# Kernel optimization log

Measured on AMD Instinct MI355X. Metric: run time of the kernel, lower is better.

## Reference

```python
import jax, jax.numpy as jnp
import numpy as np

VOCAB = 49408
D = 768
H = 12
DH = D // H
FF = 3072
L = 4
B = 32
S = 512
EPS = 1e-6


def _pos_encoding(seq_len, d):
    pos = np.arange(seq_len, dtype=np.float64)[:, None]
    j = np.arange(d, dtype=np.float64)[None, :]
    ang = pos / np.power(10000.0, 2.0 * (j // 2) / d)
    pe = np.where((np.arange(d) % 2) == 0, np.sin(ang), np.cos(ang))
    return jnp.asarray(pe, dtype=jnp.float32)  # [seq_len, d]


def _layernorm(x, g, b):
    m = jnp.mean(x, axis=-1, keepdims=True)
    v = jnp.mean(jnp.square(x - m), axis=-1, keepdims=True)
    return g * (x - m) * jax.lax.rsqrt(v + EPS) + b


def setup_inputs() -> dict:
    key = jax.random.key(0)
    ks = jax.random.split(key, 16)
    s = 0.02
    inp = {
        "tokens": jax.random.randint(ks[0], (B, S), 0, VOCAB, dtype=jnp.int32),
        "emb": jax.random.normal(ks[1], (VOCAB, D), jnp.float32) * s,
        "wq": jax.random.normal(ks[2], (L, D, D), jnp.float32) * s,
        "bq": jnp.zeros((L, D), jnp.float32),
        "wk": jax.random.normal(ks[3], (L, D, D), jnp.float32) * s,
        "bk": jnp.zeros((L, D), jnp.float32),
        "wv": jax.random.normal(ks[4], (L, D, D), jnp.float32) * s,
        "bv": jnp.zeros((L, D), jnp.float32),
        "wo": jax.random.normal(ks[5], (L, D, D), jnp.float32) * s,
        "bo": jnp.zeros((L, D), jnp.float32),
        "w1": jax.random.normal(ks[6], (L, D, FF), jnp.float32) * s,
        "b1": jnp.zeros((L, FF), jnp.float32),
        "w2": jax.random.normal(ks[7], (L, FF, D), jnp.float32) * s,
        "b2": jnp.zeros((L, D), jnp.float32),
        "ln1_g": jnp.ones((L, D), jnp.float32),
        "ln1_b": jnp.zeros((L, D), jnp.float32),
        "ln2_g": jnp.ones((L, D), jnp.float32),
        "ln2_b": jnp.zeros((L, D), jnp.float32),
        "wl": jax.random.normal(ks[8], (D, 32), jnp.float32) * s,
        "bl": jnp.zeros((32,), jnp.float32),
        "wout": jax.random.normal(ks[9], (32, 1), jnp.float32) * s,
        "bout": jnp.zeros((1,), jnp.float32),
    }
    return inp


def reference(tokens, emb, wq, bq, wk, bk, wv, bv, wo, bo, w1, b1, w2, b2,
              ln1_g, ln1_b, ln2_g, ln2_b, wl, bl, wout, bout):
    seq_len = tokens.shape[1]
    pe = _pos_encoding(seq_len, D)  # [S, D] constant
    x = emb[tokens] * jnp.sqrt(jnp.float32(D)) + pe[None, :, :]  # [B,S,D]
    scale = 1.0 / jnp.sqrt(jnp.float32(DH))
    for i in range(L):
        # multi-head attention (naive full score matrix, mask=None)
        q = (jnp.einsum('bsd,de->bse', x, wq[i]) + bq[i]).reshape(-1, seq_len, H, DH)
        k = (jnp.einsum('bsd,de->bse', x, wk[i]) + bk[i]).reshape(-1, seq_len, H, DH)
        v = (jnp.einsum('bsd,de->bse', x, wv[i]) + bv[i]).reshape(-1, seq_len, H, DH)
        scores = jnp.einsum('bqhd,bkhd->bhqk', q, k) * scale  # [B,H,S,S]
        attn = jax.nn.softmax(scores, axis=-1)
        av = jnp.einsum('bhqk,bkhd->bqhd', attn, v).reshape(-1, seq_len, D)
        attn_out = jnp.einsum('bsd,de->bse', av, wo[i]) + bo[i]
        out1 = _layernorm(x + attn_out, ln1_g[i], ln1_b[i])
        # FFN: relu -> dense
        h = jax.nn.relu(jnp.einsum('bsd,df->bsf', out1, w1[i]) + b1[i])
        ffn = jnp.einsum('bsf,fd->bsd', h, w2[i]) + b2[i]
        x = _layernorm(out1 + ffn, ln2_g[i], ln2_b[i])
    pooled = jnp.mean(x, axis=1)  # GlobalAveragePooling1D -> [B,D]
    h = jax.nn.gelu(pooled @ wl + bl, approximate=False)
    out = jax.nn.sigmoid(h @ wout + bout)  # [B,1]
    return out
```

## Files before the change

kernel.cpp:

```cpp
#include <hip/hip_runtime.h>
#include <hip/hip_bf16.h>
#include <math.h>


#define B_  32
#define S_  512
#define D_  768
#define H_  12
#define DH_ 64
#define FF_ 3072
#define L_  4
#define QKVSTR 2304

typedef __attribute__((ext_vector_type(8))) short short8;
typedef __attribute__((ext_vector_type(4))) short short4v;
typedef __attribute__((ext_vector_type(4))) float f32x4;

__device__ __forceinline__ void async16(const void* g, void* l) {
    __builtin_amdgcn_global_load_lds(
        (const __attribute__((address_space(1))) void*)g,
        (__attribute__((address_space(3))) void*)l, 16, 0, 0);
}

__device__ __forceinline__ ushort f2bf(float f) {
    __hip_bfloat16 h = __float2bfloat16(f);
    return __builtin_bit_cast(ushort, h);
}

__device__ __forceinline__ short8 scale8_eighth(short8 v) {
    short8 r;
#pragma unroll
    for (int e = 0; e < 8; e++) {
        ushort u = (ushort)v[e];
        ushort ex = u & 0x7f80;
        r[e] = (short)(ex > 0x0180 ? (ushort)(u - 0x0180) : (ushort)(u & 0x8000));
    }
    return r;
}

__global__ void pe_kernel(float* __restrict__ pe) {
    int idx = blockIdx.x * 256 + threadIdx.x;
    if (idx >= S_ * D_) return;
    int s = idx / D_, j = idx % D_;
    double e = (2.0 * (double)(j >> 1)) / (double)D_;
    double denom = pow(10000.0, e);
    double ang = (double)s / denom;
    pe[idx] = (j & 1) ? (float)cos(ang) : (float)sin(ang);
}

__global__ void embed_kernel(const int* __restrict__ tokens,
                             const float* __restrict__ emb,
                             const float* __restrict__ pe,
                             float* __restrict__ x,
                             __hip_bfloat16* __restrict__ xb) {
    int row = blockIdx.x;
    int s = row & (S_ - 1);
    int tok = tokens[row];
    float scale = sqrtf((float)D_);
    for (int i = threadIdx.x; i < D_; i += 256) {
        float v = emb[(size_t)tok * D_ + i] * scale + pe[s * D_ + i];
        x[(size_t)row * D_ + i] = v;
        xb[(size_t)row * D_ + i] = __float2bfloat16(v);
    }
}

__global__ __launch_bounds__(256) void transpose_bf16_l(
    const float* __restrict__ in, __hip_bfloat16* __restrict__ out,
    int R, int C, size_t inL, size_t outL)
{
    __shared__ float tile[32][33];
    in  += (size_t)blockIdx.z * inL;
    out += (size_t)blockIdx.z * outL;
    int tx = threadIdx.x & 31, ty = threadIdx.x >> 5;
    int c0 = blockIdx.x * 32, r0 = blockIdx.y * 32;
#pragma unroll
    for (int d = 0; d < 32; d += 8)
        tile[ty + d][tx] = in[(size_t)(r0 + ty + d) * C + c0 + tx];
    __syncthreads();
#pragma unroll
    for (int d = 0; d < 32; d += 8)
        out[(size_t)(c0 + ty + d) * R + r0 + tx] = __float2bfloat16(tile[tx][ty + d]);
}

__global__ void biascat(const float* __restrict__ bq, const float* __restrict__ bk,
                        const float* __restrict__ bv, float* __restrict__ o) {
    int i = blockIdx.x * 256 + threadIdx.x;
    int ll = i / QKVSTR, j = i % QKVSTR;
    o[i] = j < 768 ? bq[ll * 768 + j]
         : j < 1536 ? bk[ll * 768 + j - 768]
                    : bv[ll * 768 + j - 1536];
}

#define BAR()   __builtin_amdgcn_s_barrier()
#define LGKM0() asm volatile("s_waitcnt lgkmcnt(0)" ::: "memory")
#define VM4()   asm volatile("s_waitcnt vmcnt(4)" ::: "memory")

#define STAGE_A(buf, h, kt) do { \
    async16(aSrc[h][0] + (kt) * 64, &lds[(buf) * 2][dOff[h][0]]); \
    async16(aSrc[h][1] + (kt) * 64, &lds[(buf) * 2][dOff[h][1]]); } while (0)
#define STAGE_B(buf, h, kt) do { \
    async16(bSrc[h][0] + (kt) * 64, &lds[(buf) * 2 + 1][dOff[h][0]]); \
    async16(bSrc[h][1] + (kt) * 64, &lds[(buf) * 2 + 1][dOff[h][1]]); } while (0)

#define LDA(buf, m, ks) (*(const short8*)((const char*)(&lds[(buf) * 2][0]) + \
    (size_t)((arow + (m) * 16) * 128 + cswz[ks])))
#define LDB(buf, n, ks) (*(const short8*)((const char*)(&lds[(buf) * 2 + 1][0]) + \
    (size_t)((brow + (n) * 16) * 128 + cswz[ks])))

#define MFMA_Q(mh, nh) do { \
    __builtin_amdgcn_s_setprio(1); \
    _Pragma("unroll") \
    for (int ks_ = 0; ks_ < 2; ks_++) { \
      _Pragma("unroll") \
      for (int n_ = 0; n_ < 2; n_++) { \
        _Pragma("unroll") \
        for (int m_ = 0; m_ < 4; m_++) { \
          acc[(mh) * 4 + m_][(nh) * 2 + n_] = \
              __builtin_amdgcn_mfma_f32_16x16x32_bf16( \
                  a[m_][ks_], b[(nh) * 2 + n_][ks_], \
                  acc[(mh) * 4 + m_][(nh) * 2 + n_], 0, 0, 0); \
        } } } \
    __builtin_amdgcn_s_setprio(0); \
} while (0)

template<int RELU>
__global__ __launch_bounds__(512, 2) void gemm256(
    const ushort* __restrict__ A,
    const ushort* __restrict__ Bt,
    const float* __restrict__ bias,
    __hip_bfloat16* __restrict__ C,
    int M, int N, int K, int NX)
{
    __shared__ alignas(16) ushort lds[4][16384];

    int t = threadIdx.x;
    int l = t & 63, w = t >> 6;
    int wmi = w >> 2, wni = w & 3;
    int lm = l & 15, lo = l >> 4;

    int nwg = gridDim.x;
    int bid = blockIdx.x;
    int lid = (nwg & 7) ? bid : ((bid & 7) * (nwg >> 3) + (bid >> 3));
    int bn = lid % NX, bm = lid / NX;
    int row0 = bm << 8, col0 = bn << 8;

    const ushort* aSrc[2][2];
    const ushort* bSrc[2][2];
    int dOff[2][2];
#pragma unroll
    for (int h = 0; h < 2; h++) {
#pragma unroll
        for (int c = 0; c < 2; c++) {
            int p = h * 16384 + c * 8192 + t * 16;
            int prow = p >> 7;
            int scolb = (p & 127) ^ ((prow & 7) << 4);
            dOff[h][c] = p >> 1;
            aSrc[h][c] = A  + (size_t)(row0 + prow) * K + (scolb >> 1);
            bSrc[h][c] = Bt + (size_t)(col0 + prow) * K + (scolb >> 1);
        }
    }

    int arow = wmi * 128 + lm;
    int brow = wni * 64 + lm;
    int swz = (lm & 7) << 4;
    int cswz[2];
    cswz[0] = (lo * 16) ^ swz;
    cswz[1] = (64 + lo * 16) ^ swz;

    f32x4 acc[8][4];
#pragma unroll
    for (int i = 0; i < 8; i++)
#pragma unroll
        for (int j = 0; j < 4; j++) acc[i][j] = (f32x4){0.f, 0.f, 0.f, 0.f};
    short8 a[4][2], b[4][2];

    const int NK = K >> 6;
    const int NI = NK >> 1;

    STAGE_A(0, 0, 0); STAGE_A(0, 1, 0);
    STAGE_B(0, 0, 0); STAGE_B(0, 1, 0);
    STAGE_B(1, 0, 1); STAGE_B(1, 1, 1);
    VM4();
    BAR();

    for (int i = 0; i < NI; i++) {
        int kt  = 2 * i;
        int ktA = (kt + 2 <= NK - 2) ? kt + 2 : NK - 2;
        int ktB = (kt + 3 <= NK - 1) ? kt + 3 : NK - 1;

#pragma unroll
        for (int m = 0; m < 4; m++) { a[m][0] = LDA(0, m, 0); a[m][1] = LDA(0, m, 1); }
#pragma unroll
        for (int n = 0; n < 2; n++) { b[n][0] = LDB(0, n, 0); b[n][1] = LDB(0, n, 1); }
        STAGE_A(1, 0, kt + 1);
        BAR(); LGKM0();
        MFMA_Q(0, 0);
        BAR();

#pragma unroll
        for (int n = 0; n < 2; n++) { b[2 + n][0] = LDB(0, 2 + n, 0); b[2 + n][1] = LDB(0, 2 + n, 1); }
        STAGE_A(1, 1, kt + 1);
        BAR(); LGKM0();
        MFMA_Q(0, 1);
        BAR();

#pragma unroll
        for (int m = 0; m < 4; m++) { a[m][0] = LDA(0, 4 + m, 0); a[m][1] = LDA(0, 4 + m, 1); }
        STAGE_B(0, 0, ktA);
        BAR(); LGKM0();
        MFMA_Q(1, 0);
        BAR();

        STAGE_B(0, 1, ktA);
        BAR(); LGKM0();
        MFMA_Q(1, 1);
        VM4();
        BAR();

#pragma unroll
        for (int m = 0; m < 4; m++) { a[m][0] = LDA(1, m, 0); a[m][1] = LDA(1, m, 1); }
#pragma unroll
        for (int n = 0; n < 2; n++) { b[n][0] = LDB(1, n, 0); b[n][1] = LDB(1, n, 1); }
        STAGE_A(0, 0, ktA);
        BAR(); LGKM0();
        MFMA_Q(0, 0);
        BAR();

#pragma unroll
        for (int n = 0; n < 2; n++) { b[2 + n][0] = LDB(1, 2 + n, 0); b[2 + n][1] = LDB(1, 2 + n, 1); }
        STAGE_A(0, 1, ktA);
        BAR(); LGKM0();
        MFMA_Q(0, 1);
        BAR();

#pragma unroll
        for (int m = 0; m < 4; m++) { a[m][0] = LDA(1, 4 + m, 0); a[m][1] = LDA(1, 4 + m, 1); }
        STAGE_B(1, 0, ktB);
        BAR(); LGKM0();
        MFMA_Q(1, 0);
        BAR();

        STAGE_B(1, 1, ktB);
        BAR(); LGKM0();
        MFMA_Q(1, 1);
        VM4();
        BAR();
    }

    int crow = row0 + wmi * 128;
    int ccol = col0 + wni * 64;
#pragma unroll
    for (int n = 0; n < 4; n++) {
        int c = ccol + n * 16 + lm;
        float bs = bias[c];
#pragma unroll
        for (int m = 0; m < 8; m++) {
#pragma unroll
            for (int r = 0; r < 4; r++) {
                float v = acc[m][n][r] + bs;
                if (RELU) v = fmaxf(v, 0.f);
                C[(size_t)(crow + m * 16 + lo * 4 + r) * N + c] = __float2bfloat16(v);
            }
        }
    }
    (void)M;
}

#define PSTR 72
__global__ __launch_bounds__(256) void attn_mfma(
    const ushort* __restrict__ qkv,
    __hip_bfloat16* __restrict__ av)
{
    __shared__ alignas(16) ushort sQP[128 * PSTR];
    __shared__ alignas(16) ushort sK[64 * PSTR];
    __shared__ alignas(16) ushort sVt[64 * PSTR];

    int t = threadIdx.x;
    int qt = blockIdx.x, h = blockIdx.y, b = blockIdx.z;
    int w = t >> 6, l = t & 63;
    int lm = l & 15, lq = l >> 4;
    int wm = w * 32;

    const ushort* qbase = qkv + (size_t)(b * S_ + qt * 128) * QKVSTR + h * DH_;
    const ushort* kbase = qkv + (size_t)b * S_ * QKVSTR + 768 + h * DH_;
    const ushort* vbase = qkv + (size_t)b * S_ * QKVSTR + 1536 + h * DH_;

    {
        int r = t >> 1, c0 = (t & 1) * 32;
        const ushort* src = qbase + (size_t)r * QKVSTR + c0;
        ushort* dst = &sQP[r * PSTR + c0];
        *(uint4*)(dst + 0)  = *(const uint4*)(src + 0);
        *(uint4*)(dst + 8)  = *(const uint4*)(src + 8);
        *(uint4*)(dst + 16) = *(const uint4*)(src + 16);
        *(uint4*)(dst + 24) = *(const uint4*)(src + 24);
    }
    __syncthreads();
    short8 qf[2][2];
#pragma unroll
    for (int i = 0; i < 2; i++)
#pragma unroll
        for (int ks = 0; ks < 2; ks++)
            qf[i][ks] = scale8_eighth(
                *(const short8*)&sQP[(wm + i * 16 + lm) * PSTR + ks * 32 + lq * 8]);

    ushort* sPw = &sQP[(size_t)wm * PSTR];

    f32x4 accO[4][2];
    float mrun[2], lrun[2];
#pragma unroll
    for (int dk = 0; dk < 4; dk++)
#pragma unroll
        for (int i = 0; i < 2; i++) accO[dk][i] = (f32x4){0.f, 0.f, 0.f, 0.f};
    mrun[0] = mrun[1] = -1e30f;
    lrun[0] = lrun[1] = 0.f;

    for (int kt = 0; kt < S_ / 64; kt++) {
        __syncthreads();
        {
            int r = t >> 2, c0 = (t & 3) * 16;
            const ushort* ksrc = kbase + (size_t)(kt * 64 + r) * QKVSTR + c0;
            ushort* kdst = &sK[r * PSTR + c0];
            *(uint4*)(kdst + 0) = *(const uint4*)(ksrc + 0);
            *(uint4*)(kdst + 8) = *(const uint4*)(ksrc + 8);
            int p = t & 31, d0 = (t >> 5) * 8;
            const ushort* vsrc = vbase + (size_t)(kt * 64 + 2 * p) * QKVSTR + d0;
            uint4 v0 = *(const uint4*)(vsrc);
            uint4 v1 = *(const uint4*)(vsrc + QKVSTR);
            const ushort* e0 = (const ushort*)&v0;
            const ushort* e1 = (const ushort*)&v1;
#pragma unroll
            for (int j = 0; j < 8; j++) {
                uint pk = (uint)e0[j] | ((uint)e1[j] << 16);
                *(uint*)&sVt[(d0 + j) * PSTR + 2 * p] = pk;
            }
        }
        __syncthreads();

        f32x4 accS[4][2];
#pragma unroll
        for (int sb = 0; sb < 4; sb++)
#pragma unroll
            for (int i = 0; i < 2; i++) accS[sb][i] = (f32x4){0.f, 0.f, 0.f, 0.f};
#pragma unroll
        for (int ks = 0; ks < 2; ks++) {
#pragma unroll
            for (int sb = 0; sb < 4; sb++) {
                short8 kf = *(const short8*)&sK[(sb * 16 + lm) * PSTR + ks * 32 + lq * 8];
#pragma unroll
                for (int i = 0; i < 2; i++)
                    accS[sb][i] = __builtin_amdgcn_mfma_f32_16x16x32_bf16(
                        kf, qf[i][ks], accS[sb][i], 0, 0, 0);
            }
        }

        float pmax[2];
#pragma unroll
        for (int i = 0; i < 2; i++) {
            float m0 = accS[0][i][0];
#pragma unroll
            for (int sb = 0; sb < 4; sb++)
#pragma unroll
                for (int r = 0; r < 4; r++) m0 = fmaxf(m0, accS[sb][i][r]);
            m0 = fmaxf(m0, __shfl_xor(m0, 16));
            m0 = fmaxf(m0, __shfl_xor(m0, 32));
            pmax[i] = m0;
        }
        float alpha[2];
#pragma unroll
        for (int i = 0; i < 2; i++) {
            float mn = fmaxf(mrun[i], pmax[i]);
            alpha[i] = __expf(mrun[i] - mn);
            mrun[i] = mn;
        }
        float rsum[2] = {0.f, 0.f};
#pragma unroll
        for (int sb = 0; sb < 4; sb++)
#pragma unroll
            for (int i = 0; i < 2; i++)
#pragma unroll
                for (int r = 0; r < 4; r++) {
                    float p = __expf(accS[sb][i][r] - mrun[i]);
                    accS[sb][i][r] = p;
                    rsum[i] += p;
                }
#pragma unroll
        for (int i = 0; i < 2; i++) {
            rsum[i] += __shfl_xor(rsum[i], 16);
            rsum[i] += __shfl_xor(rsum[i], 32);
            lrun[i] = lrun[i] * alpha[i] + rsum[i];
        }

#pragma unroll
        for (int dk = 0; dk < 4; dk++)
#pragma unroll
            for (int i = 0; i < 2; i++)
#pragma unroll
                for (int r = 0; r < 4; r++) accO[dk][i][r] *= alpha[i];

#pragma unroll
        for (int i = 0; i < 2; i++)
#pragma unroll
            for (int sb = 0; sb < 4; sb++) {
                short4v pk;
#pragma unroll
                for (int r = 0; r < 4; r++) pk[r] = (short)f2bf(accS[sb][i][r]);
                *(short4v*)&sPw[(i * 16 + lm) * PSTR + sb * 16 + lq * 4] = pk;
            }

#pragma unroll
        for (int ks = 0; ks < 2; ks++) {
            short8 pf[2];
#pragma unroll
            for (int i = 0; i < 2; i++)
                pf[i] = *(const short8*)&sPw[(i * 16 + lm) * PSTR + ks * 32 + lq * 8];
#pragma unroll
            for (int dk = 0; dk < 4; dk++) {
                short8 vf = *(const short8*)&sVt[(dk * 16 + lm) * PSTR + ks * 32 + lq * 8];
#pragma unroll
                for (int i = 0; i < 2; i++)
                    accO[dk][i] = __builtin_amdgcn_mfma_f32_16x16x32_bf16(
                        vf, pf[i], accO[dk][i], 0, 0, 0);
            }
        }
    }

    float invl[2];
    invl[0] = 1.0f / lrun[0];
    invl[1] = 1.0f / lrun[1];
#pragma unroll
    for (int i = 0; i < 2; i++) {
        int row = qt * 128 + wm + i * 16 + lm;
        __hip_bfloat16* dst = av + (size_t)(b * S_ + row) * D_ + h * DH_;
#pragma unroll
        for (int dk = 0; dk < 4; dk++) {
            short4v ok;
#pragma unroll
            for (int r = 0; r < 4; r++) ok[r] = (short)f2bf(accO[dk][i][r] * invl[i]);
            *(short4v*)(dst + dk * 16 + lq * 4) = ok;
        }
    }
}

__global__ __launch_bounds__(256) void add_ln(float* __restrict__ x,
    __hip_bfloat16* __restrict__ xb,
    const __hip_bfloat16* __restrict__ r, const float* __restrict__ g,
    const float* __restrict__ bta)
{
    __shared__ float sred[256];
    int row = blockIdx.x, t = threadIdx.x;
    size_t base = (size_t)row * D_;
    float v0 = x[base + t]       + __bfloat162float(r[base + t]);
    float v1 = x[base + t + 256] + __bfloat162float(r[base + t + 256]);
    float v2 = x[base + t + 512] + __bfloat162float(r[base + t + 512]);
    sred[t] = v0 + v1 + v2;
    __syncthreads();
    for (int o = 128; o > 0; o >>= 1) { if (t < o) sred[t] += sred[t + o]; __syncthreads(); }
    float mean = sred[0] * (1.0f / D_);
    __syncthreads();
    float d0 = v0 - mean, d1 = v1 - mean, d2 = v2 - mean;
    sred[t] = d0 * d0 + d1 * d1 + d2 * d2;
    __syncthreads();
    for (int o = 128; o > 0; o >>= 1) { if (t < o) sred[t] += sred[t + o]; __syncthreads(); }
    float rstd = rsqrtf(sred[0] * (1.0f / D_) + 1e-6f);
    float o0 = g[t]       * d0 * rstd + bta[t];
    float o1 = g[t + 256] * d1 * rstd + bta[t + 256];
    float o2 = g[t + 512] * d2 * rstd + bta[t + 512];
    x[base + t]       = o0;
    x[base + t + 256] = o1;
    x[base + t + 512] = o2;
    xb[base + t]       = __float2bfloat16(o0);
    xb[base + t + 256] = __float2bfloat16(o1);
    xb[base + t + 512] = __float2bfloat16(o2);
}

__global__ void pool_kernel(const float* __restrict__ x, float* __restrict__ pooled) {
    int idx = blockIdx.x * 256 + threadIdx.x;
    int b = idx / D_, d = idx % D_;
    float acc = 0.f;
    const float* p = x + (size_t)b * S_ * D_ + d;
    for (int s = 0; s < S_; s++) acc += p[(size_t)s * D_];
    pooled[idx] = acc * (1.0f / S_);
}

__global__ void head_kernel(const float* __restrict__ pooled,
                            const float* __restrict__ wl,
                            const float* __restrict__ bl,
                            const float* __restrict__ wout,
                            const float* __restrict__ bout,
                            float* __restrict__ out)
{
    __shared__ float hb[32];
    int b = blockIdx.x, t = threadIdx.x;
    if (t < 32) {
        float z = bl[t];
        for (int d = 0; d < D_; d++) z += pooled[b * D_ + d] * wl[d * 32 + t];
        hb[t] = 0.5f * z * (1.0f + erff(z * 0.70710678118654752f));
    }
    __syncthreads();
    if (t == 0) {
        float z = bout[0];
        for (int j = 0; j < 32; j++) z += hb[j] * wout[j];
        out[b] = 1.0f / (1.0f + expf(-z));
    }
}

extern "C" void kernel_launch(void* const* d_in, const int* in_sizes, int n_in,
                              void* d_out, int out_size, void* d_ws, size_t ws_size,
                              hipStream_t stream)
{
    (void)in_sizes; (void)n_in; (void)out_size; (void)ws_size;
    const int*   tokens = (const int*)  d_in[0];
    const float* emb    = (const float*)d_in[1];
    const float* wq     = (const float*)d_in[2];
    const float* bq     = (const float*)d_in[3];
    const float* wk     = (const float*)d_in[4];
    const float* bk     = (const float*)d_in[5];
    const float* wv     = (const float*)d_in[6];
    const float* bv     = (const float*)d_in[7];
    const float* wo     = (const float*)d_in[8];
    const float* bo     = (const float*)d_in[9];
    const float* w1     = (const float*)d_in[10];
    const float* b1     = (const float*)d_in[11];
    const float* w2     = (const float*)d_in[12];
    const float* b2     = (const float*)d_in[13];
    const float* ln1g   = (const float*)d_in[14];
    const float* ln1b   = (const float*)d_in[15];
    const float* ln2g   = (const float*)d_in[16];
    const float* ln2b   = (const float*)d_in[17];
    const float* wl     = (const float*)d_in[18];
    const float* bl     = (const float*)d_in[19];
    const float* wout   = (const float*)d_in[20];
    const float* bout   = (const float*)d_in[21];
    float* out = (float*)d_out;

    char* ws = (char*)d_ws;
    size_t off = 0;
    auto alloc = [&](size_t n) -> void* {
        char* p = ws + off;
        off = (off + n + 255) & ~(size_t)255;
        return (void*)p;
    };
    const size_t XBYTES = (size_t)B_ * S_ * D_ * 4;
    const size_t XBF    = XBYTES / 2;
    float*          pe     = (float*)alloc((size_t)S_ * D_ * 4);
    float*          x      = (float*)alloc(XBYTES);
    __hip_bfloat16* xb     = (__hip_bfloat16*)alloc(XBF);
    __hip_bfloat16* r_bf   = (__hip_bfloat16*)alloc(XBF);
    char*           arena  = (char*)alloc(4 * XBF);
    __hip_bfloat16* qkv_bf = (__hip_bfloat16*)arena;
    __hip_bfloat16* av_bf  = (__hip_bfloat16*)(arena + 3 * XBF);
    __hip_bfloat16* h_bf   = (__hip_bfloat16*)arena;
    __hip_bfloat16* wT     = (__hip_bfloat16*)alloc((size_t)L_ * 7077888 * 2);
    float*          qkvbias= (float*)alloc((size_t)L_ * QKVSTR * 4);
    float*          pooled = (float*)alloc((size_t)B_ * D_ * 4);

    const int M = B_ * S_;
    const size_t DD = (size_t)D_ * D_;
    const size_t DF = (size_t)D_ * FF_;
    const size_t LSTRIDE = 4 * DD + 2 * DF;

    transpose_bf16_l<<<dim3(D_ / 32, D_ / 32, L_), 256, 0, stream>>>(
        wq, wT + 0 * DD, D_, D_, DD, LSTRIDE);
    transpose_bf16_l<<<dim3(D_ / 32, D_ / 32, L_), 256, 0, stream>>>(
        wk, wT + 1 * DD, D_, D_, DD, LSTRIDE);
    transpose_bf16_l<<<dim3(D_ / 32, D_ / 32, L_), 256, 0, stream>>>(
        wv, wT + 2 * DD, D_, D_, DD, LSTRIDE);
    transpose_bf16_l<<<dim3(D_ / 32, D_ / 32, L_), 256, 0, stream>>>(
        wo, wT + 3 * DD, D_, D_, DD, LSTRIDE);
    transpose_bf16_l<<<dim3(FF_ / 32, D_ / 32, L_), 256, 0, stream>>>(
        w1, wT + 4 * DD, D_, FF_, DF, LSTRIDE);
    transpose_bf16_l<<<dim3(D_ / 32, FF_ / 32, L_), 256, 0, stream>>>(
        w2, wT + 4 * DD + DF, FF_, D_, DF, LSTRIDE);
    biascat<<<(L_ * QKVSTR) / 256, 256, 0, stream>>>(bq, bk, bv, qkvbias);

    pe_kernel<<<(S_ * D_ + 255) / 256, 256, 0, stream>>>(pe);
    embed_kernel<<<M, 256, 0, stream>>>(tokens, emb, pe, x, xb);

    for (int l = 0; l < L_; l++) {
        __hip_bfloat16* wl_base = wT + (size_t)l * LSTRIDE;
        const ushort* qkvT = (const ushort*)(wl_base + 0 * DD);
        const ushort* woT  = (const ushort*)(wl_base + 3 * DD);
        const ushort* w1T  = (const ushort*)(wl_base + 4 * DD);
        const ushort* w2T  = (const ushort*)(wl_base + 4 * DD + DF);

        gemm256<0><<<dim3((QKVSTR / 256) * (M / 256)), 512, 0, stream>>>(
            (const ushort*)xb, qkvT, qkvbias + (size_t)l * QKVSTR, qkv_bf,
            M, QKVSTR, D_, QKVSTR / 256);

        attn_mfma<<<dim3(S_ / 128, H_, B_), 256, 0, stream>>>(
            (const ushort*)qkv_bf, av_bf);

        gemm256<0><<<dim3((D_ / 256) * (M / 256)), 512, 0, stream>>>(
            (const ushort*)av_bf, woT, bo + l * D_, r_bf, M, D_, D_, D_ / 256);
        add_ln<<<M, 256, 0, stream>>>(x, xb, r_bf, ln1g + l * D_, ln1b + l * D_);

        gemm256<1><<<dim3((FF_ / 256) * (M / 256)), 512, 0, stream>>>(
            (const ushort*)xb, w1T, b1 + l * FF_, h_bf, M, FF_, D_, FF_ / 256);
        gemm256<0><<<dim3((D_ / 256) * (M / 256)), 512, 0, stream>>>(
            (const ushort*)h_bf, w2T, b2 + l * D_, r_bf, M, D_, FF_, D_ / 256);
        add_ln<<<M, 256, 0, stream>>>(x, xb, r_bf, ln2g + l * D_, ln2b + l * D_);
    }

    pool_kernel<<<(B_ * D_) / 256, 256, 0, stream>>>(x, pooled);
    head_kernel<<<B_, 64, 0, stream>>>(pooled, wl, bl, wout, bout, out);
}
```

Measured before the change: 1.963 ms.

## Drop fp32 residual stream and stage GEMM epilogue through LDS for coalesced stores

Removes the fp32 copy of the residual activation x, keeping only the bf16 copy, so add_ln, embed and pooling read and write half the bytes. add_ln now loads packed bf16 pairs and writes bf16 in place. The GEMM epilogue writes the tile into LDS and then stores 16-byte coalesced rows instead of scattered 2-byte stores. This needs a full vmcnt(0) wait before the epilogue, and keeping the residual in bf16 lowers its precision across layers.

```diff
diff --git a/kernel.cpp b/kernel.cpp
--- a/kernel.cpp
+++ b/kernel.cpp
@@ -26,6 +26,8 @@
     __hip_bfloat16 h = __float2bfloat16(f);
     return __builtin_bit_cast(ushort, h);
 }
+__device__ __forceinline__ float bflo(uint u) { return __uint_as_float(u << 16); }
+__device__ __forceinline__ float bfhi(uint u) { return __uint_as_float(u & 0xffff0000u); }
 
 __device__ __forceinline__ short8 scale8_eighth(short8 v) {
     short8 r;
@@ -51,7 +53,6 @@
 __global__ void embed_kernel(const int* __restrict__ tokens,
                              const float* __restrict__ emb,
                              const float* __restrict__ pe,
-                             float* __restrict__ x,
                              __hip_bfloat16* __restrict__ xb) {
     int row = blockIdx.x;
     int s = row & (S_ - 1);
@@ -59,7 +60,6 @@
     float scale = sqrtf((float)D_);
     for (int i = threadIdx.x; i < D_; i += 256) {
         float v = emb[(size_t)tok * D_ + i] * scale + pe[s * D_ + i];
-        x[(size_t)row * D_ + i] = v;
         xb[(size_t)row * D_ + i] = __float2bfloat16(v);
     }
 }
@@ -94,6 +94,7 @@
 #define BAR()   __builtin_amdgcn_s_barrier()
 #define LGKM0() asm volatile("s_waitcnt lgkmcnt(0)" ::: "memory")
 #define VM4()   asm volatile("s_waitcnt vmcnt(4)" ::: "memory")
+#define VM0()   asm volatile("s_waitcnt vmcnt(0)" ::: "memory")
 
 #define STAGE_A(buf, h, kt) do { \
     async16(aSrc[h][0] + (kt) * 64, &lds[(buf) * 2][dOff[h][0]]); \
@@ -243,25 +244,37 @@
         STAGE_B(1, 1, ktB);
         BAR(); LGKM0();
         MFMA_Q(1, 1);
-        VM4();
-        BAR();
-    }
-
-    int crow = row0 + wmi * 128;
-    int ccol = col0 + wni * 64;
-#pragma unroll
-    for (int n = 0; n < 4; n++) {
-        int c = ccol + n * 16 + lm;
-        float bs = bias[c];
-#pragma unroll
-        for (int m = 0; m < 8; m++) {
-#pragma unroll
-            for (int r = 0; r < 4; r++) {
-                float v = acc[m][n][r] + bs;
-                if (RELU) v = fmaxf(v, 0.f);
-                C[(size_t)(crow + m * 16 + lo * 4 + r) * N + c] = __float2bfloat16(v);
+        VM0();
+        BAR();
+    }
+
+    ushort* eL = &lds[0][0];
+    {
+        int crow = wmi * 128;
+        int ccol = wni * 64;
+#pragma unroll
+        for (int n = 0; n < 4; n++) {
+            int c = ccol + n * 16 + lm;
+            float bs = bias[col0 + c];
+#pragma unroll
+            for (int m = 0; m < 8; m++) {
+#pragma unroll
+                for (int r = 0; r < 4; r++) {
+                    float v = acc[m][n][r] + bs;
+                    if (RELU) v = fmaxf(v, 0.f);
+                    eL[(crow + m * 16 + lo * 4 + r) * 256 + c] = f2bf(v);
+                }
             }
         }
+    }
+    __syncthreads();
+#pragma unroll
+    for (int i = 0; i < 16; i++) {
+        int byteoff = i * 8192 + t * 16;
+        int rr = byteoff >> 9;
+        int cc = (byteoff & 511) >> 1;
+        uint4 v = *(const uint4*)((const char*)eL + byteoff);
+        *(uint4*)(C + (size_t)(row0 + rr) * N + col0 + cc) = v;
     }
     (void)M;
 }
@@ -441,44 +454,58 @@
     }
 }
 
-__global__ __launch_bounds__(256) void add_ln(float* __restrict__ x,
+__global__ __launch_bounds__(256) void add_ln(
     __hip_bfloat16* __restrict__ xb,
     const __hip_bfloat16* __restrict__ r, const float* __restrict__ g,
     const float* __restrict__ bta)
 {
     __shared__ float sred[256];
     int row = blockIdx.x, t = threadIdx.x;
-    size_t base = (size_t)row * D_;
-    float v0 = x[base + t]       + __bfloat162float(r[base + t]);
-    float v1 = x[base + t + 256] + __bfloat162float(r[base + t + 256]);
-    float v2 = x[base + t + 512] + __bfloat162float(r[base + t + 512]);
-    sred[t] = v0 + v1 + v2;
+    uint* xu = (uint*)(xb + (size_t)row * D_);
+    const uint* ru = (const uint*)(r + (size_t)row * D_);
+    uint ux0 = xu[t], ur0 = ru[t];
+    float a0 = bflo(ux0) + bflo(ur0);
+    float a1 = bfhi(ux0) + bfhi(ur0);
+    float a2 = 0.f, a3 = 0.f;
+    if (t < 128) {
+        uint ux1 = xu[256 + t], ur1 = ru[256 + t];
+        a2 = bflo(ux1) + bflo(ur1);
+        a3 = bfhi(ux1) + bfhi(ur1);
+    }
+    sred[t] = a0 + a1 + a2 + a3;
     __syncthreads();
     for (int o = 128; o > 0; o >>= 1) { if (t < o) sred[t] += sred[t + o]; __syncthreads(); }
     float mean = sred[0] * (1.0f / D_);
     __syncthreads();
-    float d0 = v0 - mean, d1 = v1 - mean, d2 = v2 - mean;
-    sred[t] = d0 * d0 + d1 * d1 + d2 * d2;
+    float d0 = a0 - mean, d1 = a1 - mean;
+    float d2 = a2 - mean, d3 = a3 - mean;
+    sred[t] = d0 * d0 + d1 * d1 + (t < 128 ? d2 * d2 + d3 * d3 : 0.f);
     __syncthreads();
     for (int o = 128; o > 0; o >>= 1) { if (t < o) sred[t] += sred[t + o]; __syncthreads(); }
     float rstd = rsqrtf(sred[0] * (1.0f / D_) + 1e-6f);
-    float o0 = g[t]       * d0 * rstd + bta[t];
-    float o1 = g[t + 256] * d1 * rstd + bta[t + 256];
-    float o2 = g[t + 512] * d2 * rstd + bta[t + 512];
-    x[base + t]       = o0;
-    x[base + t + 256] = o1;
-    x[base + t + 512] = o2;
-    xb[base + t]       = __float2bfloat16(o0);
-    xb[base + t + 256] = __float2bfloat16(o1);
-    xb[base + t + 512] = __float2bfloat16(o2);
-}
-
-__global__ void pool_kernel(const float* __restrict__ x, float* __restrict__ pooled) {
+    {
+        float2 gv = ((const float2*)g)[t];
+        float2 bv = ((const float2*)bta)[t];
+        float o0 = gv.x * d0 * rstd + bv.x;
+        float o1 = gv.y * d1 * rstd + bv.y;
+        xu[t] = (uint)f2bf(o0) | ((uint)f2bf(o1) << 16);
+    }
+    if (t < 128) {
+        float2 gv = ((const float2*)g)[256 + t];
+        float2 bv = ((const float2*)bta)[256 + t];
+        float o2 = gv.x * d2 * rstd + bv.x;
+        float o3 = gv.y * d3 * rstd + bv.y;
+        xu[256 + t] = (uint)f2bf(o2) | ((uint)f2bf(o3) << 16);
+    }
+}
+
+__global__ void pool_kernel(const __hip_bfloat16* __restrict__ xb,
+                            float* __restrict__ pooled) {
     int idx = blockIdx.x * 256 + threadIdx.x;
     int b = idx / D_, d = idx % D_;
     float acc = 0.f;
-    const float* p = x + (size_t)b * S_ * D_ + d;
-    for (int s = 0; s < S_; s++) acc += p[(size_t)s * D_];
+    const __hip_bfloat16* p = xb + (size_t)b * S_ * D_ + d;
+    for (int s = 0; s < S_; s++) acc += __bfloat162float(p[(size_t)s * D_]);
     pooled[idx] = acc * (1.0f / S_);
 }
 
@@ -543,7 +570,6 @@
     const size_t XBYTES = (size_t)B_ * S_ * D_ * 4;
     const size_t XBF    = XBYTES / 2;
     float*          pe     = (float*)alloc((size_t)S_ * D_ * 4);
-    float*          x      = (float*)alloc(XBYTES);
     __hip_bfloat16* xb     = (__hip_bfloat16*)alloc(XBF);
     __hip_bfloat16* r_bf   = (__hip_bfloat16*)alloc(XBF);
     char*           arena  = (char*)alloc(4 * XBF);
@@ -574,7 +600,7 @@
     biascat<<<(L_ * QKVSTR) / 256, 256, 0, stream>>>(bq, bk, bv, qkvbias);
 
     pe_kernel<<<(S_ * D_ + 255) / 256, 256, 0, stream>>>(pe);
-    embed_kernel<<<M, 256, 0, stream>>>(tokens, emb, pe, x, xb);
+    embed_kernel<<<M, 256, 0, stream>>>(tokens, emb, pe, xb);
 
     for (int l = 0; l < L_; l++) {
         __hip_bfloat16* wl_base = wT + (size_t)l * LSTRIDE;
@@ -592,15 +618,15 @@
 
         gemm256<0><<<dim3((D_ / 256) * (M / 256)), 512, 0, stream>>>(
             (const ushort*)av_bf, woT, bo + l * D_, r_bf, M, D_, D_, D_ / 256);
-        add_ln<<<M, 256, 0, stream>>>(x, xb, r_bf, ln1g + l * D_, ln1b + l * D_);
+        add_ln<<<M, 256, 0, stream>>>(xb, r_bf, ln1g + l * D_, ln1b + l * D_);
 
         gemm256<1><<<dim3((FF_ / 256) * (M / 256)), 512, 0, stream>>>(
             (const ushort*)xb, w1T, b1 + l * FF_, h_bf, M, FF_, D_, FF_ / 256);
         gemm256<0><<<dim3((D_ / 256) * (M / 256)), 512, 0, stream>>>(
             (const ushort*)h_bf, w2T, b2 + l * D_, r_bf, M, D_, FF_, D_ / 256);
-        add_ln<<<M, 256, 0, stream>>>(x, xb, r_bf, ln2g + l * D_, ln2b + l * D_);
-    }
-
-    pool_kernel<<<(B_ * D_) / 256, 256, 0, stream>>>(x, pooled);
+        add_ln<<<M, 256, 0, stream>>>(xb, r_bf, ln2g + l * D_, ln2b + l * D_);
+    }
+
+    pool_kernel<<<(B_ * D_) / 256, 256, 0, stream>>>(xb, pooled);
     head_kernel<<<B_, 64, 0, stream>>>(pooled, wl, bl, wout, bout, out);
 }
```

Result: no change. 1.936 ms (-1.4%).
